# Kernel optimization log

Measured on AMD Instinct MI355X. Metric: run time of the kernel, lower is better.

## Reference

```python
import jax, jax.numpy as jnp
import numpy as np

B, S, HID = 2, 2048, 2048
H, KVH, D = 16, 4, 128
GROUPS = H // KVH
THETA = 10000.0
SCALE = 1.0 / np.sqrt(D).astype(np.float32)
NEG = -1e9


def setup_inputs() -> dict:
    key = jax.random.key(0)
    ks = jax.random.split(key, 6)
    x = jax.random.normal(ks[0], (B, S, HID), dtype=jnp.float32)
    # causal additive mask, broadcast over heads
    causal = jnp.triu(jnp.full((S, S), NEG, dtype=jnp.float32), k=1)
    attn_mask = jnp.broadcast_to(causal, (B, 1, S, S))
    pos_ids = jnp.broadcast_to(jnp.arange(S, dtype=jnp.int32), (B, S))
    sd = 0.02
    Wq = jax.random.normal(ks[1], (H * D, HID), dtype=jnp.float32) * sd
    Wk = jax.random.normal(ks[2], (KVH * D, HID), dtype=jnp.float32) * sd
    Wv = jax.random.normal(ks[3], (KVH * D, HID), dtype=jnp.float32) * sd
    Wo = jax.random.normal(ks[4], (HID, H * D), dtype=jnp.float32) * sd
    return {"x": x, "attn_mask": attn_mask, "pos_ids": pos_ids,
            "Wq": Wq, "Wk": Wk, "Wv": Wv, "Wo": Wo}


def _rope_cos_sin(pos_ids):
    # pos_ids: [B, S] -> cos/sin: [B, 1, S, D]
    inv_freq = 1.0 / (THETA ** (jnp.arange(0, D, 2, dtype=jnp.float32) / D))
    freqs = pos_ids.astype(jnp.float32)[:, :, None] * inv_freq  # [B, S, D/2]
    emb = jnp.concatenate([freqs, freqs], axis=-1)              # [B, S, D]
    return jnp.cos(emb)[:, None], jnp.sin(emb)[:, None]


def _rotate_half(t):
    t1, t2 = jnp.split(t, 2, axis=-1)
    return jnp.concatenate([-t2, t1], axis=-1)


def reference(x, attn_mask, pos_ids, Wq, Wk, Wv, Wo):
    b, s, _ = x.shape
    q = jnp.einsum('bsh,oh->bso', x, Wq).reshape(b, s, H, D).transpose(0, 2, 1, 3)
    k = jnp.einsum('bsh,oh->bso', x, Wk).reshape(b, s, KVH, D).transpose(0, 2, 1, 3)
    v = jnp.einsum('bsh,oh->bso', x, Wv).reshape(b, s, KVH, D).transpose(0, 2, 1, 3)
    cos, sin = _rope_cos_sin(pos_ids)
    q = q * cos + _rotate_half(q) * sin
    k = k * cos + _rotate_half(k) * sin
    # GQA: repeat kv heads
    k = jnp.repeat(k, GROUPS, axis=1)  # [b, H, s, D]
    v = jnp.repeat(v, GROUPS, axis=1)
    scores = jnp.einsum('bhqd,bhkd->bhqk', q, k) * SCALE + attn_mask
    weights = jax.nn.softmax(scores, axis=-1)  # dropout p=0 (eval)
    out = jnp.einsum('bhqk,bhkd->bhqd', weights, v)
    out = out.transpose(0, 2, 1, 3).reshape(b, s, H * D)
    return jnp.einsum('bso,ho->bsh', out, Wo)
```

## Files before the change

### kernel.cpp

```cpp
#include <hip/hip_runtime.h>
#include <hip/hip_bf16.h>
#include <stdint.h>

#define B_   2
#define S_   2048
#define HID_ 2048
#define H_   16
#define KVH_ 4
#define D_   128
#define SCALE_ 0.08838834764831845f
#define QSC_ (SCALE_ * 1.4426950408889634f)

typedef __attribute__((ext_vector_type(8))) short bf16x8;
typedef __attribute__((ext_vector_type(4))) float f32x4;
typedef __attribute__((ext_vector_type(4))) short short4v;

__device__ __forceinline__ void async_copy16(void* lds, const void* g) {
  __builtin_amdgcn_global_load_lds((__attribute__((address_space(1))) void*)(uintptr_t)g,
                                   (__attribute__((address_space(3))) void*)lds, 16, 0, 0);
}

__device__ __forceinline__ short bf16bits(float f) {
  __hip_bfloat16 t = __float2bfloat16(f);
  return __builtin_bit_cast(short, t);
}
__device__ __forceinline__ float bf16tof(short s) {
  return __bfloat162float(__builtin_bit_cast(__hip_bfloat16, s));
}

__global__ __launch_bounds__(256) void f2b_all(const float4* __restrict__ x,
                                               const float4* __restrict__ wq,
                                               const float4* __restrict__ wk,
                                               const float4* __restrict__ wv,
                                               const float4* __restrict__ wo,
                                               short4v* __restrict__ xb,
                                               short4v* __restrict__ wqb,
                                               short4v* __restrict__ wkb,
                                               short4v* __restrict__ wvb,
                                               short4v* __restrict__ wob) {
  int i = blockIdx.x * blockDim.x + threadIdx.x;
  const float4* src; short4v* dst; int off;
  if (i < 2097152)      { src = x;  dst = xb;  off = 0; }
  else if (i < 3145728) { src = wq; dst = wqb; off = 2097152; }
  else if (i < 3407872) { src = wk; dst = wkb; off = 3145728; }
  else if (i < 3670016) { src = wv; dst = wvb; off = 3407872; }
  else                  { src = wo; dst = wob; off = 3670016; }
  int k = i - off;
  float4 v = src[k];
  short4v o;
  o[0] = bf16bits(v.x); o[1] = bf16bits(v.y);
  o[2] = bf16bits(v.z); o[3] = bf16bits(v.w);
  dst[k] = o;
}

__global__ __launch_bounds__(256) void gemm_qkv(const __hip_bfloat16* __restrict__ A,
                                                const __hip_bfloat16* __restrict__ Bw,
                                                __hip_bfloat16* __restrict__ Qo,
                                                __hip_bfloat16* __restrict__ Ko,
                                                __hip_bfloat16* __restrict__ Vo) {
  __shared__ __align__(16) __hip_bfloat16 Asm[256 * 64];
  __shared__ __align__(16) __hip_bfloat16 Bsm[96 * 64];
  const int tid  = threadIdx.x;
  const int lane = tid & 63;
  const int wid  = tid >> 6;
  const int id  = blockIdx.y * 32 + blockIdx.x;
  const int swz = (id & 7) * 64 + (id >> 3);
  const int m0 = (swz >> 5) * 256;
  const int n0 = (swz & 31) * 96;
  const int qm = wid * 64;
  const int ar = lane & 15;
  const int ag = lane >> 4;

  f32x4 acc[4][6] = {};

  for (int k0 = 0; k0 < 2048; k0 += 64) {
#pragma unroll
    for (int c = 0; c < 8; ++c) {
      const int idx = c * 256 + tid;
      const int row = idx >> 3;
      const int cu  = (idx & 7) ^ (row & 7);
      async_copy16(&Asm[idx * 8], A + (size_t)(m0 + row) * 2048 + k0 + cu * 8);
    }
#pragma unroll
    for (int c = 0; c < 3; ++c) {
      const int idx = c * 256 + tid;
      const int row = idx >> 3;
      const int cu  = (idx & 7) ^ (row & 7);
      async_copy16(&Bsm[idx * 8], Bw + (size_t)(n0 + row) * 2048 + k0 + cu * 8);
    }
    __syncthreads();

#pragma unroll
    for (int kk = 0; kk < 2; ++kk) {
      bf16x8 af[4], bfr[6];
#pragma unroll
      for (int i = 0; i < 4; ++i) {
        const int row = qm + i * 16 + ar;
        const int u = (kk * 4 + ag) ^ (row & 7);
        af[i] = *(const bf16x8*)(&Asm[row * 64 + u * 8]);
      }
#pragma unroll
      for (int j = 0; j < 6; ++j) {
        const int row = j * 16 + ar;
        const int u = (kk * 4 + ag) ^ (row & 7);
        bfr[j] = *(const bf16x8*)(&Bsm[row * 64 + u * 8]);
      }
#pragma unroll
      for (int i = 0; i < 4; ++i)
#pragma unroll
        for (int j = 0; j < 6; ++j)
          acc[i][j] = __builtin_amdgcn_mfma_f32_16x16x32_bf16(af[i], bfr[j], acc[i][j], 0, 0, 0);
    }
    __syncthreads();
  }

  const int rb = (lane >> 4) * 4;
  const int cl = lane & 15;
#pragma unroll
  for (int i = 0; i < 4; ++i)
#pragma unroll
    for (int j = 0; j < 6; ++j) {
      const int n = n0 + j * 16 + cl;
#pragma unroll
      for (int r = 0; r < 4; ++r) {
        const int m = m0 + qm + i * 16 + rb + r;
        const float v = acc[i][j][r];
        const int bb = m >> 11, ss = m & (S_ - 1);
        if (n < 2048) {
          const int hh = n >> 7, dd = n & 127;
          Qo[(((size_t)bb * 16 + hh) * S_ + ss) * D_ + dd] = __float2bfloat16(v);
        } else if (n < 2560) {
          const int n2 = n - 2048, hh = n2 >> 7, dd = n2 & 127;
          Ko[(((size_t)bb * 4 + hh) * S_ + ss) * D_ + dd] = __float2bfloat16(v);
        } else {
          const int n2 = n - 2560, hh = n2 >> 7, dd = n2 & 127;
          Vo[(((size_t)bb * 4 + hh) * D_ + dd) * S_ + ss] = __float2bfloat16(v);
        }
      }
    }
}

__global__ __launch_bounds__(256) void gemm_out(const __hip_bfloat16* __restrict__ A,
                                                const __hip_bfloat16* __restrict__ Bw,
                                                float* __restrict__ Cout,
                                                int M, int N, int K) {
  __shared__ __align__(16) __hip_bfloat16 Asm[2][128 * 64];
  __shared__ __align__(16) __hip_bfloat16 Bsm[2][128 * 64];
  const int tid  = threadIdx.x;
  const int lane = tid & 63;
  const int wid  = tid >> 6;
  const int nwg = gridDim.x * gridDim.y;
  const int id  = blockIdx.y * gridDim.x + blockIdx.x;
  const int swz = (id & 7) * (nwg >> 3) + (id >> 3);
  const int m0 = (swz / gridDim.x) * 128;
  const int n0 = (swz % gridDim.x) * 128;
  const int qm = (wid >> 1) * 64;
  const int qn = (wid & 1) * 64;
  const int ar = lane & 15;
  const int ag = lane >> 4;
  const int srow = tid >> 3;
  const int sun  = tid & 7;

  auto STAGE = [&](int sb, int k0) {
#pragma unroll
    for (int c = 0; c < 4; ++c) {
      const int row = c * 32 + srow;
      const int cu  = sun ^ (row & 7);
      async_copy16(&Asm[sb][c * 2048 + tid * 8], A  + (size_t)(m0 + row) * K + k0 + cu * 8);
      async_copy16(&Bsm[sb][c * 2048 + tid * 8], Bw + (size_t)(n0 + row) * K + k0 + cu * 8);
    }
  };

  f32x4 acc[4][4] = {};

  auto COMPUTE = [&](int sb) {
#pragma unroll
    for (int kk = 0; kk < 2; ++kk) {
      bf16x8 af[4], bfr[4];
#pragma unroll
      for (int i = 0; i < 4; ++i) {
        const int row = qm + i * 16 + ar;
        const int u = (kk * 4 + ag) ^ (row & 7);
        af[i] = *(const bf16x8*)(&Asm[sb][row * 64 + u * 8]);
      }
#pragma unroll
      for (int j = 0; j < 4; ++j) {
        const int row = qn + j * 16 + ar;
        const int u = (kk * 4 + ag) ^ (row & 7);
        bfr[j] = *(const bf16x8*)(&Bsm[sb][row * 64 + u * 8]);
      }
#pragma unroll
      for (int i = 0; i < 4; ++i)
#pragma unroll
        for (int j = 0; j < 4; ++j)
          acc[i][j] = __builtin_amdgcn_mfma_f32_16x16x32_bf16(af[i], bfr[j], acc[i][j], 0, 0, 0);
    }
  };

  STAGE(0, 0);
  int cur = 0;
  for (int k0 = 0; k0 < K; k0 += 64) {
    if (k0 + 64 < K) {
      STAGE(cur ^ 1, k0 + 64);
      asm volatile("s_waitcnt vmcnt(8)" ::: "memory");
    } else {
      asm volatile("s_waitcnt vmcnt(0)" ::: "memory");
    }
    __builtin_amdgcn_s_barrier();
    COMPUTE(cur);
    __builtin_amdgcn_s_barrier();
    cur ^= 1;
  }

  const int rb = (lane >> 4) * 4;
  const int cl = lane & 15;
#pragma unroll
  for (int i = 0; i < 4; ++i)
#pragma unroll
    for (int j = 0; j < 4; ++j) {
      const int n = n0 + qn + j * 16 + cl;
#pragma unroll
      for (int r = 0; r < 4; ++r) {
        const int m = m0 + qm + i * 16 + rb + r;
        Cout[(size_t)m * N + n] = acc[i][j][r];
      }
    }
}

__global__ __launch_bounds__(256) void rope_all(__hip_bfloat16* __restrict__ qb,
                                                __hip_bfloat16* __restrict__ kb,
                                                const int* __restrict__ pos_ids) {
  int idx = blockIdx.x * blockDim.x + threadIdx.x;
  __hip_bfloat16* buf;
  float scale;
  int b, rel;
  if (idx < 1048576) {
    rel = idx; buf = qb; scale = QSC_; b = (rel >> 15) >> 4;
  } else {
    rel = idx - 1048576; buf = kb; scale = 1.0f; b = (rel >> 15) >> 2;
  }
  const int t  = rel & 15;
  const int s  = (rel >> 4) & (S_ - 1);
  const int bh = rel >> 15;
  float pos = (float)pos_ids[b * S_ + s];
  size_t base = ((size_t)bh * S_ + s) * D_ + t * 4;
  short4v lo = *(short4v*)(buf + base);
  short4v hi = *(short4v*)(buf + base + 64);
  short4v lo2, hi2;
#pragma unroll
  for (int e = 0; e < 4; ++e) {
    float d = (float)(t * 4 + e);
    float ang = pos * exp2f(d * -0.20762050593046014f);
    float c = cosf(ang), sn = sinf(ang);
    float lv = bf16tof(lo[e]), hv = bf16tof(hi[e]);
    lo2[e] = bf16bits((lv * c - hv * sn) * scale);
    hi2[e] = bf16bits((hv * c + lv * sn) * scale);
  }
  *(short4v*)(buf + base)      = lo2;
  *(short4v*)(buf + base + 64) = hi2;
}

__global__ __launch_bounds__(256, 2) void flash_attn7(const __hip_bfloat16* __restrict__ Q,
                                                      const __hip_bfloat16* __restrict__ K,
                                                      const __hip_bfloat16* __restrict__ Vt,
                                                      __hip_bfloat16* __restrict__ O) {
  __shared__ __align__(16) __hip_bfloat16 Ksm[2][64 * 128];
  __shared__ __align__(16) __hip_bfloat16 Vsm[2][128 * 64];
  __shared__ __align__(16) __hip_bfloat16 Psm[4][16 * 64];
  const int lane = threadIdx.x & 63;
  const int wid  = threadIdx.x >> 6;
  const int i   = blockIdx.x;
  const int xcd = i & 7;
  const int j   = i >> 3;
  const int bh  = xcd * 4 + (j & 3);
  const int qt  = 31 - (j >> 2);
  const int b   = bh >> 4;
  const int h   = bh & 15;
  const int kvh = h >> 2;
  const int qrow0 = qt * 64 + wid * 16;
  const int ar = lane & 15;
  const int ag = lane >> 4;
  const int q  = qrow0 + ar;
  const int nkv = qt + 1;

  const __hip_bfloat16* Qb = Q  + ((size_t)bh * S_ + qrow0) * D_;
  const __hip_bfloat16* Kb = K  + (size_t)(b * KVH_ + kvh) * S_ * D_;
  const __hip_bfloat16* Vb = Vt + (size_t)(b * KVH_ + kvh) * D_ * S_;

  bf16x8 qf[4];
#pragma unroll
  for (int kf = 0; kf < 4; ++kf)
    qf[kf] = *(const bf16x8*)(Qb + (size_t)ar * D_ + kf * 32 + ag * 8);

  auto STAGE = [&](int sb, int t) {
    const int kv0 = t * 64;
#pragma unroll
    for (int c = 0; c < 4; ++c) {
      const int idx = wid * 4 + c;
      const int rowK = idx * 4 + (lane >> 4);
      const int gcK  = (lane & 15) ^ (rowK & 7);
      async_copy16(&Ksm[sb][idx * 512 + lane * 8],
                   Kb + (size_t)(kv0 + rowK) * D_ + gcK * 8);
      const int rowV = idx * 8 + (lane >> 3);
      const int gcV  = (lane & 7) ^ (rowV & 7);
      async_copy16(&Vsm[sb][idx * 512 + lane * 8],
                   Vb + (size_t)rowV * S_ + kv0 + gcV * 8);
    }
  };

  f32x4 acc[8] = {};
  float l = 0.f;
  char* pb = (char*)&Psm[wid][0];

  STAGE(0, 0);
  asm volatile("s_waitcnt vmcnt(0)" ::: "memory");
  __syncthreads();

  int buf = 0;
  for (int t = 0; t < nkv; ++t, buf ^= 1) {
    if (t + 1 < nkv) STAGE(buf ^ 1, t + 1);
    const int kv0 = t * 64;
    f32x4 st[4] = {};
    const char* kbase = (const char*)&Ksm[buf][0];
    __builtin_amdgcn_s_setprio(1);
#pragma unroll
    for (int kvt = 0; kvt < 4; ++kvt) {
      const int rr = kvt * 16 + ar;
      const int rx = rr & 7;
#pragma unroll
      for (int kf = 0; kf < 4; ++kf) {
        const bf16x8 kfrag = *(const bf16x8*)(kbase + rr * 256 + (((kf * 4 + ag) ^ rx) << 4));
        st[kvt] = __builtin_amdgcn_mfma_f32_16x16x32_bf16(kfrag, qf[kf], st[kvt], 0, 0, 0);
      }
    }
    __builtin_amdgcn_s_setprio(0);
    const bool needmask = (t == nkv - 1);
    float psum = 0.f;
#pragma unroll
    for (int kvt = 0; kvt < 4; ++kvt) {
      short4v pk;
#pragma unroll
      for (int r = 0; r < 4; ++r) {
        float s = st[kvt][r];
        if (needmask && (kv0 + kvt * 16 + ag * 4 + r > q)) s = -3.0e38f;
        const float p = exp2f(s - 8.f);
        psum += p;
        pk[r] = bf16bits(p);
      }
      const int g = kvt * 2 + (ag >> 1);
      *(short4v*)(pb + ar * 128 + ((g ^ (ar & 7)) << 4) + (ag & 1) * 8) = pk;
    }
    psum += __shfl_xor(psum, 16, 64);
    psum += __shfl_xor(psum, 32, 64);
    l += psum;
    asm volatile("s_waitcnt lgkmcnt(0)" ::: "memory");
    const bf16x8 pf0 = *(const bf16x8*)(pb + ar * 128 + ((ag ^ (ar & 7)) << 4));
    const bf16x8 pf1 = *(const bf16x8*)(pb + ar * 128 + (((4 + ag) ^ (ar & 7)) << 4));
    const char* vbase = (const char*)&Vsm[buf][0];
    __builtin_amdgcn_s_setprio(1);
#pragma unroll
    for (int df = 0; df < 8; ++df) {
      const int rr = df * 16 + ar;
      const int rx = rr & 7;
      const bf16x8 v0 = *(const bf16x8*)(vbase + rr * 128 + ((ag ^ rx) << 4));
      const bf16x8 v1 = *(const bf16x8*)(vbase + rr * 128 + (((4 + ag) ^ rx) << 4));
      acc[df] = __builtin_amdgcn_mfma_f32_16x16x32_bf16(v0, pf0, acc[df], 0, 0, 0);
      acc[df] = __builtin_amdgcn_mfma_f32_16x16x32_bf16(v1, pf1, acc[df], 0, 0, 0);
    }
    __builtin_amdgcn_s_setprio(0);
    asm volatile("s_waitcnt vmcnt(0)" ::: "memory");
    __syncthreads();
  }

  const float linv = 1.f / l;
  __hip_bfloat16* Ob = O + ((size_t)b * S_ + qrow0 + ar) * (H_ * D_) + h * D_;
#pragma unroll
  for (int df = 0; df < 8; ++df) {
    short4v o4;
#pragma unroll
    for (int r = 0; r < 4; ++r)
      o4[r] = bf16bits(acc[df][r] * linv);
    *(short4v*)(Ob + df * 16 + ag * 4) = o4;
  }
}

extern "C" void kernel_launch(void* const* d_in, const int* in_sizes, int n_in,
                              void* d_out, int out_size, void* d_ws, size_t ws_size,
                              hipStream_t stream) {
  (void)in_sizes; (void)n_in; (void)out_size; (void)ws_size;
  const float* x  = (const float*)d_in[0];
  const int* pos  = (const int*)d_in[2];
  const float* Wq = (const float*)d_in[3];
  const float* Wk = (const float*)d_in[4];
  const float* Wv = (const float*)d_in[5];
  const float* Wo = (const float*)d_in[6];

  char* ws = (char*)d_ws;
  __hip_bfloat16* xb   = (__hip_bfloat16*)(ws);
  __hip_bfloat16* wqb  = (__hip_bfloat16*)(ws + 16777216);
  __hip_bfloat16* wkb  = (__hip_bfloat16*)(ws + 25165824);
  __hip_bfloat16* wvb  = (__hip_bfloat16*)(ws + 27262976);
  __hip_bfloat16* wob  = (__hip_bfloat16*)(ws + 29360128);
  __hip_bfloat16* qb16 = (__hip_bfloat16*)(ws + 37748736);
  __hip_bfloat16* kb16 = (__hip_bfloat16*)(ws + 54525952);
  __hip_bfloat16* vt16 = (__hip_bfloat16*)(ws + 58720256);
  __hip_bfloat16* attn = (__hip_bfloat16*)(ws + 62914560);

  f2b_all<<<18432, 256, 0, stream>>>((const float4*)x, (const float4*)Wq, (const float4*)Wk,
                                     (const float4*)Wv, (const float4*)Wo,
                                     (short4v*)xb, (short4v*)wqb, (short4v*)wkb,
                                     (short4v*)wvb, (short4v*)wob);

  gemm_qkv<<<dim3(32, 16), 256, 0, stream>>>(xb, wqb, qb16, kb16, vt16);

  rope_all<<<5120, 256, 0, stream>>>(qb16, kb16, pos);

  flash_attn7<<<1024, 256, 0, stream>>>(qb16, kb16, vt16, attn);

  gemm_out<<<dim3(16, 32), 256, 0, stream>>>(attn, wob, (float*)d_out, 4096, 2048, 2048);
}
```

Baseline: 202.5 us.

## Double-buffer QKV GEMM with async LDS prefetch and 128x192 tiles

Rewrites the QKV projection GEMM so global-to-LDS copies for the next K-slice are issued while the current slice is computed, using two LDS buffers and explicit vmcnt waits in place of full syncthreads. The block tile also changes from 256x96 to 128x192 with a 2x2 wave layout, which alters per-wave A/B reuse. The goal is to hide global load latency behind MFMA work. In exchange, LDS use rises to 80KB per block, which may cut occupancy, and correctness relies on the hand-counted vmcnt value.

```diff
diff --git a/kernel.cpp b/kernel.cpp
--- a/kernel.cpp
+++ b/kernel.cpp
@@ -53,43 +53,45 @@
   dst[k] = o;
 }
 
-__global__ __launch_bounds__(256) void gemm_qkv(const __hip_bfloat16* __restrict__ A,
-                                                const __hip_bfloat16* __restrict__ Bw,
-                                                __hip_bfloat16* __restrict__ Qo,
-                                                __hip_bfloat16* __restrict__ Ko,
-                                                __hip_bfloat16* __restrict__ Vo) {
-  __shared__ __align__(16) __hip_bfloat16 Asm[256 * 64];
-  __shared__ __align__(16) __hip_bfloat16 Bsm[96 * 64];
+__global__ __launch_bounds__(256) void gemm_qkv2(const __hip_bfloat16* __restrict__ A,
+                                                 const __hip_bfloat16* __restrict__ Bw,
+                                                 __hip_bfloat16* __restrict__ Qo,
+                                                 __hip_bfloat16* __restrict__ Ko,
+                                                 __hip_bfloat16* __restrict__ Vo) {
+  __shared__ __align__(16) __hip_bfloat16 Asm[2][128 * 64];
+  __shared__ __align__(16) __hip_bfloat16 Bsm[2][192 * 64];
   const int tid  = threadIdx.x;
   const int lane = tid & 63;
   const int wid  = tid >> 6;
-  const int id  = blockIdx.y * 32 + blockIdx.x;
+  const int id  = blockIdx.y * 16 + blockIdx.x;
   const int swz = (id & 7) * 64 + (id >> 3);
-  const int m0 = (swz >> 5) * 256;
-  const int n0 = (swz & 31) * 96;
-  const int qm = wid * 64;
+  const int m0 = (swz >> 4) * 128;
+  const int n0 = (swz & 15) * 192;
+  const int qm = (wid >> 1) * 64;
+  const int qn = (wid & 1) * 96;
   const int ar = lane & 15;
   const int ag = lane >> 4;
 
-  f32x4 acc[4][6] = {};
-
-  for (int k0 = 0; k0 < 2048; k0 += 64) {
-#pragma unroll
-    for (int c = 0; c < 8; ++c) {
+  auto STAGE = [&](int sb, int k0) {
+#pragma unroll
+    for (int c = 0; c < 4; ++c) {
       const int idx = c * 256 + tid;
       const int row = idx >> 3;
       const int cu  = (idx & 7) ^ (row & 7);
-      async_copy16(&Asm[idx * 8], A + (size_t)(m0 + row) * 2048 + k0 + cu * 8);
-    }
-#pragma unroll
-    for (int c = 0; c < 3; ++c) {
+      async_copy16(&Asm[sb][idx * 8], A + (size_t)(m0 + row) * 2048 + k0 + cu * 8);
+    }
+#pragma unroll
+    for (int c = 0; c < 6; ++c) {
       const int idx = c * 256 + tid;
       const int row = idx >> 3;
       const int cu  = (idx & 7) ^ (row & 7);
-      async_copy16(&Bsm[idx * 8], Bw + (size_t)(n0 + row) * 2048 + k0 + cu * 8);
-    }
-    __syncthreads();
-
+      async_copy16(&Bsm[sb][idx * 8], Bw + (size_t)(n0 + row) * 2048 + k0 + cu * 8);
+    }
+  };
+
+  f32x4 acc[4][6] = {};
+
+  auto COMPUTE = [&](int sb) {
 #pragma unroll
     for (int kk = 0; kk < 2; ++kk) {
       bf16x8 af[4], bfr[6];
@@ -97,13 +99,13 @@
       for (int i = 0; i < 4; ++i) {
         const int row = qm + i * 16 + ar;
         const int u = (kk * 4 + ag) ^ (row & 7);
-        af[i] = *(const bf16x8*)(&Asm[row * 64 + u * 8]);
+        af[i] = *(const bf16x8*)(&Asm[sb][row * 64 + u * 8]);
       }
 #pragma unroll
       for (int j = 0; j < 6; ++j) {
-        const int row = j * 16 + ar;
+        const int row = qn + j * 16 + ar;
         const int u = (kk * 4 + ag) ^ (row & 7);
-        bfr[j] = *(const bf16x8*)(&Bsm[row * 64 + u * 8]);
+        bfr[j] = *(const bf16x8*)(&Bsm[sb][row * 64 + u * 8]);
       }
 #pragma unroll
       for (int i = 0; i < 4; ++i)
@@ -111,7 +113,21 @@
         for (int j = 0; j < 6; ++j)
           acc[i][j] = __builtin_amdgcn_mfma_f32_16x16x32_bf16(af[i], bfr[j], acc[i][j], 0, 0, 0);
     }
-    __syncthreads();
+  };
+
+  STAGE(0, 0);
+  int cur = 0;
+  for (int k0 = 0; k0 < 2048; k0 += 64) {
+    if (k0 + 64 < 2048) {
+      STAGE(cur ^ 1, k0 + 64);
+      asm volatile("s_waitcnt vmcnt(10)" ::: "memory");
+    } else {
+      asm volatile("s_waitcnt vmcnt(0)" ::: "memory");
+    }
+    __builtin_amdgcn_s_barrier();
+    COMPUTE(cur);
+    __builtin_amdgcn_s_barrier();
+    cur ^= 1;
   }
 
   const int rb = (lane >> 4) * 4;
@@ -120,7 +136,7 @@
   for (int i = 0; i < 4; ++i)
 #pragma unroll
     for (int j = 0; j < 6; ++j) {
-      const int n = n0 + j * 16 + cl;
+      const int n = n0 + qn + j * 16 + cl;
 #pragma unroll
       for (int r = 0; r < 4; ++r) {
         const int m = m0 + qm + i * 16 + rb + r;
@@ -411,7 +427,7 @@
                                      (short4v*)xb, (short4v*)wqb, (short4v*)wkb,
                                      (short4v*)wvb, (short4v*)wob);
 
-  gemm_qkv<<<dim3(32, 16), 256, 0, stream>>>(xb, wqb, qb16, kb16, vt16);
+  gemm_qkv2<<<dim3(16, 32), 256, 0, stream>>>(xb, wqb, qb16, kb16, vt16);
 
   rope_all<<<5120, 256, 0, stream>>>(qb16, kb16, pos);
 
```

New measurement: 228.4 us. +12.8%, slower.

## Fuse Q RoPE into attention and retile QKV GEMM to 128x128

Applied to the files above, without the earlier changes.

Query RoPE and the softmax scale are now applied in registers inside the attention kernel right after the Q fragments load. This removes the separate read-modify-write pass over the Q buffer, and the RoPE kernel now handles only K. The QKV projection GEMM changes from 256x96 tiles to 128x128 tiles on a 2x2 wave layout with an updated block swizzle. That gives 768 blocks instead of 512, which should help occupancy and load balance. The cost is redundant sin/cos work in attention, since each Q row is rotated once per block, and the GEMM tile reuses inputs less.

```diff
diff --git a/kernel.cpp b/kernel.cpp
--- a/kernel.cpp
+++ b/kernel.cpp
@@ -58,41 +58,37 @@
                                                 __hip_bfloat16* __restrict__ Qo,
                                                 __hip_bfloat16* __restrict__ Ko,
                                                 __hip_bfloat16* __restrict__ Vo) {
-  __shared__ __align__(16) __hip_bfloat16 Asm[256 * 64];
-  __shared__ __align__(16) __hip_bfloat16 Bsm[96 * 64];
+  __shared__ __align__(16) __hip_bfloat16 Asm[128 * 64];
+  __shared__ __align__(16) __hip_bfloat16 Bsm[128 * 64];
   const int tid  = threadIdx.x;
   const int lane = tid & 63;
   const int wid  = tid >> 6;
-  const int id  = blockIdx.y * 32 + blockIdx.x;
-  const int swz = (id & 7) * 64 + (id >> 3);
-  const int m0 = (swz >> 5) * 256;
-  const int n0 = (swz & 31) * 96;
-  const int qm = wid * 64;
+  const int id  = blockIdx.y * 24 + blockIdx.x;
+  const int swz = (id & 7) * 96 + (id >> 3);
+  const int m0 = (swz / 24) * 128;
+  const int n0 = (swz % 24) * 128;
+  const int qm = (wid >> 1) * 64;
+  const int qn = (wid & 1) * 64;
   const int ar = lane & 15;
   const int ag = lane >> 4;
-
-  f32x4 acc[4][6] = {};
+  const int srow = tid >> 3;
+  const int sun  = tid & 7;
+
+  f32x4 acc[4][4] = {};
 
   for (int k0 = 0; k0 < 2048; k0 += 64) {
 #pragma unroll
-    for (int c = 0; c < 8; ++c) {
-      const int idx = c * 256 + tid;
-      const int row = idx >> 3;
-      const int cu  = (idx & 7) ^ (row & 7);
-      async_copy16(&Asm[idx * 8], A + (size_t)(m0 + row) * 2048 + k0 + cu * 8);
-    }
-#pragma unroll
-    for (int c = 0; c < 3; ++c) {
-      const int idx = c * 256 + tid;
-      const int row = idx >> 3;
-      const int cu  = (idx & 7) ^ (row & 7);
-      async_copy16(&Bsm[idx * 8], Bw + (size_t)(n0 + row) * 2048 + k0 + cu * 8);
+    for (int c = 0; c < 4; ++c) {
+      const int row = c * 32 + srow;
+      const int cu  = sun ^ (row & 7);
+      async_copy16(&Asm[c * 2048 + tid * 8], A  + (size_t)(m0 + row) * 2048 + k0 + cu * 8);
+      async_copy16(&Bsm[c * 2048 + tid * 8], Bw + (size_t)(n0 + row) * 2048 + k0 + cu * 8);
     }
     __syncthreads();
 
 #pragma unroll
     for (int kk = 0; kk < 2; ++kk) {
-      bf16x8 af[4], bfr[6];
+      bf16x8 af[4], bfr[4];
 #pragma unroll
       for (int i = 0; i < 4; ++i) {
         const int row = qm + i * 16 + ar;
@@ -100,15 +96,15 @@
         af[i] = *(const bf16x8*)(&Asm[row * 64 + u * 8]);
       }
 #pragma unroll
-      for (int j = 0; j < 6; ++j) {
-        const int row = j * 16 + ar;
+      for (int j = 0; j < 4; ++j) {
+        const int row = qn + j * 16 + ar;
         const int u = (kk * 4 + ag) ^ (row & 7);
         bfr[j] = *(const bf16x8*)(&Bsm[row * 64 + u * 8]);
       }
 #pragma unroll
       for (int i = 0; i < 4; ++i)
 #pragma unroll
-        for (int j = 0; j < 6; ++j)
+        for (int j = 0; j < 4; ++j)
           acc[i][j] = __builtin_amdgcn_mfma_f32_16x16x32_bf16(af[i], bfr[j], acc[i][j], 0, 0, 0);
     }
     __syncthreads();
@@ -119,8 +115,8 @@
 #pragma unroll
   for (int i = 0; i < 4; ++i)
 #pragma unroll
-    for (int j = 0; j < 6; ++j) {
-      const int n = n0 + j * 16 + cl;
+    for (int j = 0; j < 4; ++j) {
+      const int n = n0 + qn + j * 16 + cl;
 #pragma unroll
       for (int r = 0; r < 4; ++r) {
         const int m = m0 + qm + i * 16 + rb + r;
@@ -227,21 +223,13 @@
     }
 }
 
-__global__ __launch_bounds__(256) void rope_all(__hip_bfloat16* __restrict__ qb,
-                                                __hip_bfloat16* __restrict__ kb,
-                                                const int* __restrict__ pos_ids) {
+__global__ __launch_bounds__(256) void rope_k(__hip_bfloat16* __restrict__ buf,
+                                              const int* __restrict__ pos_ids) {
   int idx = blockIdx.x * blockDim.x + threadIdx.x;
-  __hip_bfloat16* buf;
-  float scale;
-  int b, rel;
-  if (idx < 1048576) {
-    rel = idx; buf = qb; scale = QSC_; b = (rel >> 15) >> 4;
-  } else {
-    rel = idx - 1048576; buf = kb; scale = 1.0f; b = (rel >> 15) >> 2;
-  }
-  const int t  = rel & 15;
-  const int s  = (rel >> 4) & (S_ - 1);
-  const int bh = rel >> 15;
+  const int t  = idx & 15;
+  const int s  = (idx >> 4) & (S_ - 1);
+  const int bh = idx >> 15;
+  const int b  = bh >> 2;
   float pos = (float)pos_ids[b * S_ + s];
   size_t base = ((size_t)bh * S_ + s) * D_ + t * 4;
   short4v lo = *(short4v*)(buf + base);
@@ -253,16 +241,17 @@
     float ang = pos * exp2f(d * -0.20762050593046014f);
     float c = cosf(ang), sn = sinf(ang);
     float lv = bf16tof(lo[e]), hv = bf16tof(hi[e]);
-    lo2[e] = bf16bits((lv * c - hv * sn) * scale);
-    hi2[e] = bf16bits((hv * c + lv * sn) * scale);
+    lo2[e] = bf16bits(lv * c - hv * sn);
+    hi2[e] = bf16bits(hv * c + lv * sn);
   }
   *(short4v*)(buf + base)      = lo2;
   *(short4v*)(buf + base + 64) = hi2;
 }
 
-__global__ __launch_bounds__(256, 2) void flash_attn7(const __hip_bfloat16* __restrict__ Q,
+__global__ __launch_bounds__(256, 2) void flash_attn9(const __hip_bfloat16* __restrict__ Q,
                                                       const __hip_bfloat16* __restrict__ K,
                                                       const __hip_bfloat16* __restrict__ Vt,
+                                                      const int* __restrict__ pos_ids,
                                                       __hip_bfloat16* __restrict__ O) {
   __shared__ __align__(16) __hip_bfloat16 Ksm[2][64 * 128];
   __shared__ __align__(16) __hip_bfloat16 Vsm[2][128 * 64];
@@ -292,6 +281,25 @@
   for (int kf = 0; kf < 4; ++kf)
     qf[kf] = *(const bf16x8*)(Qb + (size_t)ar * D_ + kf * 32 + ag * 8);
 
+  {
+    const float posf = (float)pos_ids[b * S_ + q];
+#pragma unroll
+    for (int kf = 0; kf < 2; ++kf) {
+      bf16x8 lo = qf[kf], hi = qf[kf + 2];
+      bf16x8 nlo, nhi;
+#pragma unroll
+      for (int e = 0; e < 8; ++e) {
+        const float d = (float)(kf * 32 + ag * 8 + e);
+        const float ang = posf * exp2f(d * -0.20762050593046014f);
+        const float c = cosf(ang), sn = sinf(ang);
+        const float lv = bf16tof(lo[e]), hv = bf16tof(hi[e]);
+        nlo[e] = bf16bits((lv * c - hv * sn) * QSC_);
+        nhi[e] = bf16bits((hv * c + lv * sn) * QSC_);
+      }
+      qf[kf] = nlo; qf[kf + 2] = nhi;
+    }
+  }
+
   auto STAGE = [&](int sb, int t) {
     const int kv0 = t * 64;
 #pragma unroll
@@ -411,11 +419,11 @@
                                      (short4v*)xb, (short4v*)wqb, (short4v*)wkb,
                                      (short4v*)wvb, (short4v*)wob);
 
-  gemm_qkv<<<dim3(32, 16), 256, 0, stream>>>(xb, wqb, qb16, kb16, vt16);
-
-  rope_all<<<5120, 256, 0, stream>>>(qb16, kb16, pos);
-
-  flash_attn7<<<1024, 256, 0, stream>>>(qb16, kb16, vt16, attn);
+  gemm_qkv<<<dim3(24, 32), 256, 0, stream>>>(xb, wqb, qb16, kb16, vt16);
+
+  rope_k<<<1024, 256, 0, stream>>>(kb16, pos);
+
+  flash_attn9<<<1024, 256, 0, stream>>>(qb16, kb16, vt16, pos, attn);
 
   gemm_out<<<dim3(16, 32), 256, 0, stream>>>(attn, wob, (float*)d_out, 4096, 2048, 2048);
 }
```

Result: slower. 220.4 us (+8.8%).
